# Kernel tuning notes

Measured on AMD Instinct MI355X. Metric: run time of the kernel, lower is better.

Reference implementation:

```python
import jax, jax.numpy as jnp
import numpy as np

B, S, D, H = 2, 4096, 512, 8
DK = D // H  # 64

def setup_inputs() -> dict:
    key = jax.random.key(0)
    k1, k2, k3, k4 = jax.random.split(key, 4)
    return {
        "queries": jax.random.normal(k1, (B, S, D), dtype=jnp.float32),
        "keys": jax.random.normal(k2, (B, S, D), dtype=jnp.float32),
        "values": jax.random.normal(k3, (B, S, D), dtype=jnp.float32),
        "W_o": jax.random.normal(k4, (D, D), dtype=jnp.float32) * (1.0 / np.sqrt(D)),
        "b_o": jnp.zeros((D,), dtype=jnp.float32),
    }

def reference(queries, keys, values, W_o, b_o):
    b_s, nq, _ = queries.shape
    nk = keys.shape[1]
    # split heads: (b, s, h, dk) -> (b, h, s, dk)
    q = queries.reshape(b_s, nq, H, DK).transpose(0, 2, 1, 3)
    k = keys.reshape(b_s, nk, H, DK).transpose(0, 2, 1, 3)
    v = values.reshape(b_s, nk, H, DK).transpose(0, 2, 1, 3)
    # full (nq, nk) attention matrix, scaled by sqrt(d_k)
    att = jnp.einsum("bhqd,bhkd->bhqk", q, k) / np.sqrt(DK).astype(np.float32)
    att = jax.nn.softmax(att, axis=-1)  # dropout is identity at inference
    out = jnp.einsum("bhqk,bhkd->bhqd", att, v)
    out = out.transpose(0, 2, 1, 3).reshape(b_s, nq, H * DK)
    return out @ W_o + b_o
```

## Files before the change

kernel.cpp:

```cpp
#include <hip/hip_runtime.h>
#include <hip/hip_bf16.h>

#define Bn 2
#define Sn 4096
#define Dn 512
#define Hn 8
#define DKn 64

typedef __bf16 bf16x8 __attribute__((ext_vector_type(8)));
typedef float f32x4 __attribute__((ext_vector_type(4)));

static __device__ __forceinline__ unsigned short f2bf(float x) {
    __hip_bfloat16 h = __float2bfloat16(x);
    return *reinterpret_cast<unsigned short*>(&h);
}

__global__ __launch_bounds__(256) void cvt_kernel(const float* __restrict__ in,
                                                  unsigned short* __restrict__ out, int n) {
    int i = (blockIdx.x * 256 + threadIdx.x) * 4;
    if (i < n) {
        float4 v = *(const float4*)(in + i);
        ushort4 o;
        o.x = f2bf(v.x); o.y = f2bf(v.y); o.z = f2bf(v.z); o.w = f2bf(v.w);
        *(ushort4*)(out + i) = o;
    }
}

__global__ __launch_bounds__(256) void vtrans_kernel(const float* __restrict__ V,
                                                     unsigned short* __restrict__ Vtb) {
    const int st = blockIdx.x;
    const int bh = blockIdx.y;
    const int b = bh >> 3, h = bh & 7;
    __shared__ unsigned short T[64][68];
    const int t = threadIdx.x;
    const int rlo = t >> 4;
    const int c4 = (t & 15) * 4;
    for (int i = 0; i < 4; ++i) {
        int row = rlo + i * 16;
        float4 v = *(const float4*)(V + ((size_t)(b * Sn + st * 64 + row)) * Dn + h * DKn + c4);
        T[row][c4 + 0] = f2bf(v.x); T[row][c4 + 1] = f2bf(v.y);
        T[row][c4 + 2] = f2bf(v.z); T[row][c4 + 3] = f2bf(v.w);
    }
    __syncthreads();
    for (int i = 0; i < 4; ++i) {
        int dk = rlo + i * 16;
        ushort4 o;
        o.x = T[c4 + 0][dk]; o.y = T[c4 + 1][dk]; o.z = T[c4 + 2][dk]; o.w = T[c4 + 3][dk];
        *(ushort4*)(Vtb + ((size_t)(bh * DKn + dk)) * Sn + st * 64 + c4) = o;
    }
}

__global__ __launch_bounds__(256) void wtrans_kernel(const float* __restrict__ W,
                                                     unsigned short* __restrict__ Wtb) {
    const int kt = blockIdx.x;
    const int nt = blockIdx.y;
    __shared__ unsigned short T[64][68];
    const int t = threadIdx.x;
    const int rlo = t >> 4;
    const int c4 = (t & 15) * 4;
    for (int i = 0; i < 4; ++i) {
        int row = rlo + i * 16;
        float4 v = *(const float4*)(W + (size_t)(kt * 64 + row) * Dn + nt * 64 + c4);
        T[row][c4 + 0] = f2bf(v.x); T[row][c4 + 1] = f2bf(v.y);
        T[row][c4 + 2] = f2bf(v.z); T[row][c4 + 3] = f2bf(v.w);
    }
    __syncthreads();
    for (int i = 0; i < 4; ++i) {
        int n = rlo + i * 16;
        ushort4 o;
        o.x = T[c4 + 0][n]; o.y = T[c4 + 1][n]; o.z = T[c4 + 2][n]; o.w = T[c4 + 3][n];
        *(ushort4*)(Wtb + (size_t)(nt * 64 + n) * Dn + kt * 64 + c4) = o;
    }
}

__global__ __launch_bounds__(256) void attn_kernel(
    const float* __restrict__ Q,
    const unsigned short* __restrict__ Kb,
    const unsigned short* __restrict__ Vtb,
    unsigned short* __restrict__ Ob) {
    __shared__ __align__(16) unsigned short Ksh[64 * 64];
    __shared__ __align__(16) unsigned short Vsh[64 * 64];
    __shared__ __align__(16) unsigned short Psh[4][16 * 64];

    const int qt = blockIdx.x;
    const int bh = blockIdx.y;
    const int b = bh >> 3, h = bh & 7;
    const int tid = threadIdx.x;
    const int w = tid >> 6;
    const int lane = tid & 63;
    const int l15 = lane & 15;
    const int quad = lane >> 4;
    const int q0 = qt * 64 + w * 16;
    const float cexp = 0.18033688f;

    bf16x8 qf[2];
    {
        const float* qp = Q + ((size_t)(b * Sn + q0 + l15)) * Dn + h * DKn + quad * 8;
        for (int ks = 0; ks < 2; ++ks) {
            float4 a0 = *(const float4*)(qp + ks * 32);
            float4 a1 = *(const float4*)(qp + ks * 32 + 4);
            union { unsigned short u[8]; bf16x8 v; } f;
            f.u[0] = f2bf(a0.x * cexp); f.u[1] = f2bf(a0.y * cexp);
            f.u[2] = f2bf(a0.z * cexp); f.u[3] = f2bf(a0.w * cexp);
            f.u[4] = f2bf(a1.x * cexp); f.u[5] = f2bf(a1.y * cexp);
            f.u[6] = f2bf(a1.z * cexp); f.u[7] = f2bf(a1.w * cexp);
            qf[ks] = f.v;
        }
    }

    f32x4 oacc[4];
    for (int n4 = 0; n4 < 4; ++n4)
        for (int r = 0; r < 4; ++r) oacc[n4][r] = 0.f;
    float l_ = 0.f;

    const unsigned short* Kbase = Kb + ((size_t)b * Sn) * Dn + h * DKn;
    const unsigned short* Vbase = Vtb + ((size_t)bh * DKn) * Sn;

    const int srow = tid >> 3;
    const int sch = tid & 7;

    for (int kt = 0; kt < Sn / 64; ++kt) {
        __syncthreads();
        for (int i = 0; i < 2; ++i) {
            int row = srow + i * 32;
            int sw = (sch ^ (row & 7)) * 8;
            uint4 kv = *(const uint4*)(Kbase + (size_t)(kt * 64 + row) * Dn + sch * 8);
            uint4 vv = *(const uint4*)(Vbase + (size_t)row * Sn + kt * 64 + sch * 8);
            *(uint4*)&Ksh[row * 64 + sw] = kv;
            *(uint4*)&Vsh[row * 64 + sw] = vv;
        }
        __syncthreads();

        f32x4 sacc[4];
        for (int c = 0; c < 4; ++c) {
            int kr = c * 16 + l15;
            const int sx = (kr & 7);
            bf16x8 ka0 = *(const bf16x8*)&Ksh[kr * 64 + ((quad ^ sx) * 8)];
            bf16x8 ka1 = *(const bf16x8*)&Ksh[kr * 64 + (((quad + 4) ^ sx) * 8)];
            f32x4 acc;
            for (int r = 0; r < 4; ++r) acc[r] = 0.f;
            acc = __builtin_amdgcn_mfma_f32_16x16x32_bf16(ka0, qf[0], acc, 0, 0, 0);
            acc = __builtin_amdgcn_mfma_f32_16x16x32_bf16(ka1, qf[1], acc, 0, 0, 0);
            sacc[c] = acc;
        }

        for (int c = 0; c < 4; ++c) {
            float p0 = __builtin_amdgcn_exp2f(sacc[c][0]);
            float p1 = __builtin_amdgcn_exp2f(sacc[c][1]);
            float p2 = __builtin_amdgcn_exp2f(sacc[c][2]);
            float p3 = __builtin_amdgcn_exp2f(sacc[c][3]);
            l_ += (p0 + p1) + (p2 + p3);
            ushort4 pk;
            pk.x = f2bf(p0); pk.y = f2bf(p1); pk.z = f2bf(p2); pk.w = f2bf(p3);
            int ch16 = ((quad >> 1) + 2 * c) ^ (l15 & 7);
            *(ushort4*)&Psh[w][l15 * 64 + ch16 * 8 + (quad & 1) * 4] = pk;
        }

        const int px = (l15 & 7);
        bf16x8 pb0 = *(const bf16x8*)&Psh[w][l15 * 64 + ((quad ^ px) * 8)];
        bf16x8 pb1 = *(const bf16x8*)&Psh[w][l15 * 64 + (((quad + 4) ^ px) * 8)];
        for (int n4 = 0; n4 < 4; ++n4) {
            int vr = n4 * 16 + l15;
            const int vx = (vr & 7);
            bf16x8 va0 = *(const bf16x8*)&Vsh[vr * 64 + ((quad ^ vx) * 8)];
            bf16x8 va1 = *(const bf16x8*)&Vsh[vr * 64 + (((quad + 4) ^ vx) * 8)];
            oacc[n4] = __builtin_amdgcn_mfma_f32_16x16x32_bf16(va0, pb0, oacc[n4], 0, 0, 0);
            oacc[n4] = __builtin_amdgcn_mfma_f32_16x16x32_bf16(va1, pb1, oacc[n4], 0, 0, 0);
        }
    }

    l_ += __shfl_xor(l_, 16);
    l_ += __shfl_xor(l_, 32);
    float li = 1.f / l_;
    unsigned short* op = Ob + (size_t)(b * Sn + q0 + l15) * Dn + h * DKn + quad * 4;
    for (int n4 = 0; n4 < 4; ++n4) {
        ushort4 o;
        o.x = f2bf(oacc[n4][0] * li); o.y = f2bf(oacc[n4][1] * li);
        o.z = f2bf(oacc[n4][2] * li); o.w = f2bf(oacc[n4][3] * li);
        *(ushort4*)(op + n4 * 16) = o;
    }
}

__global__ __launch_bounds__(256) void proj_kernel(
    const unsigned short* __restrict__ Ab,
    const unsigned short* __restrict__ Wtb,
    const float* __restrict__ bias,
    float* __restrict__ out) {
    __shared__ __align__(16) unsigned short Ash[64 * 64];
    __shared__ __align__(16) unsigned short Wsh[64 * 64];

    const int mt = blockIdx.x;
    const int nt = blockIdx.y;
    const int tid = threadIdx.x;
    const int w = tid >> 6;
    const int lane = tid & 63;
    const int l15 = lane & 15;
    const int quad = lane >> 4;

    f32x4 acc[4];
    for (int n4 = 0; n4 < 4; ++n4)
        for (int r = 0; r < 4; ++r) acc[n4][r] = 0.f;

    const int srow = tid >> 3;
    const int sch = tid & 7;

    for (int kt = 0; kt < Dn / 64; ++kt) {
        __syncthreads();
        for (int i = 0; i < 2; ++i) {
            int row = srow + i * 32;
            int sw = (sch ^ (row & 7)) * 8;
            *(uint4*)&Ash[row * 64 + sw] =
                *(const uint4*)(Ab + (size_t)(mt * 64 + row) * Dn + kt * 64 + sch * 8);
            *(uint4*)&Wsh[row * 64 + sw] =
                *(const uint4*)(Wtb + (size_t)(nt * 64 + row) * Dn + kt * 64 + sch * 8);
        }
        __syncthreads();

        int ar = w * 16 + l15;
        const int ax = (ar & 7);
        bf16x8 a0 = *(const bf16x8*)&Ash[ar * 64 + ((quad ^ ax) * 8)];
        bf16x8 a1 = *(const bf16x8*)&Ash[ar * 64 + (((quad + 4) ^ ax) * 8)];
        for (int n4 = 0; n4 < 4; ++n4) {
            int wr = n4 * 16 + l15;
            const int wx = (wr & 7);
            bf16x8 b0 = *(const bf16x8*)&Wsh[wr * 64 + ((quad ^ wx) * 8)];
            bf16x8 b1 = *(const bf16x8*)&Wsh[wr * 64 + (((quad + 4) ^ wx) * 8)];
            acc[n4] = __builtin_amdgcn_mfma_f32_16x16x32_bf16(a0, b0, acc[n4], 0, 0, 0);
            acc[n4] = __builtin_amdgcn_mfma_f32_16x16x32_bf16(a1, b1, acc[n4], 0, 0, 0);
        }
    }

    for (int n4 = 0; n4 < 4; ++n4) {
        int col = nt * 64 + n4 * 16 + l15;
        float bv = bias[col];
        for (int r = 0; r < 4; ++r) {
            int row = mt * 64 + w * 16 + quad * 4 + r;
            out[(size_t)row * Dn + col] = acc[n4][r] + bv;
        }
    }
}

extern "C" void kernel_launch(void* const* d_in, const int* in_sizes, int n_in,
                              void* d_out, int out_size, void* d_ws, size_t ws_size,
                              hipStream_t stream) {
    const float* Q = (const float*)d_in[0];
    const float* K = (const float*)d_in[1];
    const float* V = (const float*)d_in[2];
    const float* W = (const float*)d_in[3];
    const float* bo = (const float*)d_in[4];
    float* out = (float*)d_out;

    char* ws = (char*)d_ws;
    unsigned short* Kb  = (unsigned short*)(ws);
    unsigned short* Vtb = (unsigned short*)(ws + 8388608);
    unsigned short* Wtb = (unsigned short*)(ws + 16777216);
    unsigned short* Ob  = (unsigned short*)(ws + 17301504);

    cvt_kernel<<<4096, 256, 0, stream>>>(K, Kb, Bn * Sn * Dn);
    vtrans_kernel<<<dim3(Sn / 64, Bn * Hn), 256, 0, stream>>>(V, Vtb);
    wtrans_kernel<<<dim3(8, 8), 256, 0, stream>>>(W, Wtb);
    attn_kernel<<<dim3(Sn / 64, Bn * Hn), 256, 0, stream>>>(Q, Kb, Vtb, Ob);
    proj_kernel<<<dim3(128, 8), 256, 0, stream>>>(Ob, Wtb, bo, out);
}
```

Measured before the change: 216.9 us.

## Switch to 32x32x16 MFMA with fragment-ordered prepacked K/V/W/O layouts

Replaces the 16x16x32 MFMA tiles with 32x32x16 MFMA in both attention and projection. The prep kernels now write K, V, W and the attention output directly in per-lane MFMA fragment order, so shared-memory staging becomes contiguous copies without swizzling. P fragments are built in registers through a cross-half lane shuffle rather than a round trip through shared memory. Each attention block now covers 128 queries, which halves the block count (512 blocks) and may reduce occupancy and latency hiding. The V and W prep kernels read with strided scalar loads, which may make the prep step slower.

```diff
diff --git a/kernel.cpp b/kernel.cpp
--- a/kernel.cpp
+++ b/kernel.cpp
@@ -8,79 +8,102 @@
 #define DKn 64
 
 typedef __bf16 bf16x8 __attribute__((ext_vector_type(8)));
-typedef float f32x4 __attribute__((ext_vector_type(4)));
+typedef float f32x16 __attribute__((ext_vector_type(16)));
 
 static __device__ __forceinline__ unsigned short f2bf(float x) {
     __hip_bfloat16 h = __float2bfloat16(x);
     return *reinterpret_cast<unsigned short*>(&h);
 }
 
-__global__ __launch_bounds__(256) void cvt_kernel(const float* __restrict__ in,
-                                                  unsigned short* __restrict__ out, int n) {
-    int i = (blockIdx.x * 256 + threadIdx.x) * 4;
-    if (i < n) {
-        float4 v = *(const float4*)(in + i);
-        ushort4 o;
-        o.x = f2bf(v.x); o.y = f2bf(v.y); o.z = f2bf(v.z); o.w = f2bf(v.w);
-        *(ushort4*)(out + i) = o;
-    }
-}
-
-__global__ __launch_bounds__(256) void vtrans_kernel(const float* __restrict__ V,
-                                                     unsigned short* __restrict__ Vtb) {
-    const int st = blockIdx.x;
-    const int bh = blockIdx.y;
+static __device__ __forceinline__ uint2 pack4(float a, float b, float c, float d) {
+    union { ushort4 u; uint2 v; } r;
+    r.u.x = f2bf(a); r.u.y = f2bf(b); r.u.z = f2bf(c); r.u.w = f2bf(d);
+    return r.v;
+}
+
+static __device__ __forceinline__ bf16x8 xchg_frag(uint2 pg0, uint2 pg1, int hi) {
+    int sx = hi ? (int)pg0.x : (int)pg1.x;
+    int sy = hi ? (int)pg0.y : (int)pg1.y;
+    int rx = __shfl_xor(sx, 32);
+    int ry = __shfl_xor(sy, 32);
+    unsigned ox = hi ? pg1.x : pg0.x;
+    unsigned oy = hi ? pg1.y : pg0.y;
+    union { unsigned u[4]; bf16x8 v; } f;
+    f.u[0] = hi ? (unsigned)rx : ox;
+    f.u[1] = hi ? (unsigned)ry : oy;
+    f.u[2] = hi ? ox : (unsigned)rx;
+    f.u[3] = hi ? oy : (unsigned)ry;
+    return f.v;
+}
+
+__global__ __launch_bounds__(256) void kprep_kernel(const float* __restrict__ K,
+                                                    unsigned short* __restrict__ Kb) {
+    const int kt = blockIdx.x, bh = blockIdx.y;
     const int b = bh >> 3, h = bh & 7;
-    __shared__ unsigned short T[64][68];
-    const int t = threadIdx.x;
-    const int rlo = t >> 4;
-    const int c4 = (t & 15) * 4;
-    for (int i = 0; i < 4; ++i) {
-        int row = rlo + i * 16;
-        float4 v = *(const float4*)(V + ((size_t)(b * Sn + st * 64 + row)) * Dn + h * DKn + c4);
-        T[row][c4 + 0] = f2bf(v.x); T[row][c4 + 1] = f2bf(v.y);
-        T[row][c4 + 2] = f2bf(v.z); T[row][c4 + 3] = f2bf(v.w);
-    }
-    __syncthreads();
-    for (int i = 0; i < 4; ++i) {
-        int dk = rlo + i * 16;
-        ushort4 o;
-        o.x = T[c4 + 0][dk]; o.y = T[c4 + 1][dk]; o.z = T[c4 + 2][dk]; o.w = T[c4 + 3][dk];
-        *(ushort4*)(Vtb + ((size_t)(bh * DKn + dk)) * Sn + st * 64 + c4) = o;
-    }
-}
-
-__global__ __launch_bounds__(256) void wtrans_kernel(const float* __restrict__ W,
-                                                     unsigned short* __restrict__ Wtb) {
-    const int kt = blockIdx.x;
-    const int nt = blockIdx.y;
-    __shared__ unsigned short T[64][68];
-    const int t = threadIdx.x;
-    const int rlo = t >> 4;
-    const int c4 = (t & 15) * 4;
-    for (int i = 0; i < 4; ++i) {
-        int row = rlo + i * 16;
-        float4 v = *(const float4*)(W + (size_t)(kt * 64 + row) * Dn + nt * 64 + c4);
-        T[row][c4 + 0] = f2bf(v.x); T[row][c4 + 1] = f2bf(v.y);
-        T[row][c4 + 2] = f2bf(v.z); T[row][c4 + 3] = f2bf(v.w);
-    }
-    __syncthreads();
-    for (int i = 0; i < 4; ++i) {
-        int n = rlo + i * 16;
-        ushort4 o;
-        o.x = T[c4 + 0][n]; o.y = T[c4 + 1][n]; o.z = T[c4 + 2][n]; o.w = T[c4 + 3][n];
-        *(ushort4*)(Wtb + (size_t)(nt * 64 + n) * Dn + kt * 64 + c4) = o;
-    }
+    unsigned short* dst = Kb + ((size_t)bh * 64 + kt) * 4096;
+#pragma unroll
+    for (int i = 0; i < 2; ++i) {
+        int c = threadIdx.x + i * 256;
+        int f = c >> 6, ln = c & 63;
+        int ktile = f >> 2, ks = f & 3;
+        int row = ktile * 32 + (ln & 31);
+        int dk = ks * 16 + (ln >> 5) * 8;
+        const float* src = K + ((size_t)(b * Sn + kt * 64 + row)) * Dn + h * 64 + dk;
+        float4 a0 = *(const float4*)src;
+        float4 a1 = *(const float4*)(src + 4);
+        ushort4 o0; o0.x = f2bf(a0.x); o0.y = f2bf(a0.y); o0.z = f2bf(a0.z); o0.w = f2bf(a0.w);
+        ushort4 o1; o1.x = f2bf(a1.x); o1.y = f2bf(a1.y); o1.z = f2bf(a1.z); o1.w = f2bf(a1.w);
+        *(ushort4*)(dst + c * 8) = o0;
+        *(ushort4*)(dst + c * 8 + 4) = o1;
+    }
+}
+
+__global__ __launch_bounds__(256) void vprep_kernel(const float* __restrict__ V,
+                                                    unsigned short* __restrict__ Vb) {
+    const int kt = blockIdx.x, bh = blockIdx.y;
+    const int b = bh >> 3, h = bh & 7;
+    unsigned short* dst = Vb + ((size_t)bh * 64 + kt) * 4096;
+#pragma unroll
+    for (int i = 0; i < 2; ++i) {
+        int c = threadIdx.x + i * 256;
+        int f = c >> 6, ln = c & 63;
+        int dt = f >> 2, ks = f & 3;
+        int dk = dt * 32 + (ln & 31);
+        int key0 = ks * 16 + (ln >> 5) * 8;
+        const float* src = V + ((size_t)(b * Sn + kt * 64 + key0)) * Dn + h * 64 + dk;
+        ushort4 o0, o1;
+        o0.x = f2bf(src[0 * Dn]); o0.y = f2bf(src[1 * Dn]);
+        o0.z = f2bf(src[2 * Dn]); o0.w = f2bf(src[3 * Dn]);
+        o1.x = f2bf(src[4 * Dn]); o1.y = f2bf(src[5 * Dn]);
+        o1.z = f2bf(src[6 * Dn]); o1.w = f2bf(src[7 * Dn]);
+        *(ushort4*)(dst + c * 8) = o0;
+        *(ushort4*)(dst + c * 8 + 4) = o1;
+    }
+}
+
+__global__ __launch_bounds__(256) void wprep_kernel(const float* __restrict__ W,
+                                                    unsigned short* __restrict__ Wb) {
+    int c = blockIdx.x * 256 + threadIdx.x;
+    int ln = c & 63, f = c >> 6;
+    int ntile = f >> 5, ks = f & 31;
+    int n = ntile * 32 + (ln & 31);
+    int k0 = ks * 16 + (ln >> 5) * 8;
+    ushort4 o0, o1;
+    o0.x = f2bf(W[(size_t)(k0 + 0) * Dn + n]); o0.y = f2bf(W[(size_t)(k0 + 1) * Dn + n]);
+    o0.z = f2bf(W[(size_t)(k0 + 2) * Dn + n]); o0.w = f2bf(W[(size_t)(k0 + 3) * Dn + n]);
+    o1.x = f2bf(W[(size_t)(k0 + 4) * Dn + n]); o1.y = f2bf(W[(size_t)(k0 + 5) * Dn + n]);
+    o1.z = f2bf(W[(size_t)(k0 + 6) * Dn + n]); o1.w = f2bf(W[(size_t)(k0 + 7) * Dn + n]);
+    *(ushort4*)(Wb + c * 8) = o0;
+    *(ushort4*)(Wb + c * 8 + 4) = o1;
 }
 
 __global__ __launch_bounds__(256) void attn_kernel(
     const float* __restrict__ Q,
     const unsigned short* __restrict__ Kb,
-    const unsigned short* __restrict__ Vtb,
-    unsigned short* __restrict__ Ob) {
-    __shared__ __align__(16) unsigned short Ksh[64 * 64];
-    __shared__ __align__(16) unsigned short Vsh[64 * 64];
-    __shared__ __align__(16) unsigned short Psh[4][16 * 64];
+    const unsigned short* __restrict__ Vb,
+    unsigned short* __restrict__ ObA) {
+    __shared__ __align__(16) unsigned short Ksh[4096];
+    __shared__ __align__(16) unsigned short Vsh[4096];
 
     const int qt = blockIdx.x;
     const int bh = blockIdx.y;
@@ -88,17 +111,18 @@
     const int tid = threadIdx.x;
     const int w = tid >> 6;
     const int lane = tid & 63;
-    const int l15 = lane & 15;
-    const int quad = lane >> 4;
-    const int q0 = qt * 64 + w * 16;
+    const int q = lane & 31;
+    const int hi = lane >> 5;
+    const int q0 = qt * 128 + w * 32;
     const float cexp = 0.18033688f;
 
-    bf16x8 qf[2];
+    bf16x8 qf[4];
     {
-        const float* qp = Q + ((size_t)(b * Sn + q0 + l15)) * Dn + h * DKn + quad * 8;
-        for (int ks = 0; ks < 2; ++ks) {
-            float4 a0 = *(const float4*)(qp + ks * 32);
-            float4 a1 = *(const float4*)(qp + ks * 32 + 4);
+        const float* qp = Q + ((size_t)(b * Sn + q0 + q)) * Dn + h * 64 + hi * 8;
+#pragma unroll
+        for (int ks = 0; ks < 4; ++ks) {
+            float4 a0 = *(const float4*)(qp + ks * 16);
+            float4 a1 = *(const float4*)(qp + ks * 16 + 4);
             union { unsigned short u[8]; bf16x8 v; } f;
             f.u[0] = f2bf(a0.x * cexp); f.u[1] = f2bf(a0.y * cexp);
             f.u[2] = f2bf(a0.z * cexp); f.u[3] = f2bf(a0.w * cexp);
@@ -108,134 +132,146 @@
         }
     }
 
-    f32x4 oacc[4];
-    for (int n4 = 0; n4 < 4; ++n4)
-        for (int r = 0; r < 4; ++r) oacc[n4][r] = 0.f;
+    f32x16 oacc[2];
+#pragma unroll
+    for (int t = 0; t < 2; ++t)
+#pragma unroll
+        for (int r = 0; r < 16; ++r) oacc[t][r] = 0.f;
     float l_ = 0.f;
 
-    const unsigned short* Kbase = Kb + ((size_t)b * Sn) * Dn + h * DKn;
-    const unsigned short* Vbase = Vtb + ((size_t)bh * DKn) * Sn;
-
-    const int srow = tid >> 3;
-    const int sch = tid & 7;
-
-    for (int kt = 0; kt < Sn / 64; ++kt) {
+    const unsigned short* kg = Kb + (size_t)bh * (64 * 4096);
+    const unsigned short* vg = Vb + (size_t)bh * (64 * 4096);
+
+    for (int kt = 0; kt < 64; ++kt) {
         __syncthreads();
-        for (int i = 0; i < 2; ++i) {
-            int row = srow + i * 32;
-            int sw = (sch ^ (row & 7)) * 8;
-            uint4 kv = *(const uint4*)(Kbase + (size_t)(kt * 64 + row) * Dn + sch * 8);
-            uint4 vv = *(const uint4*)(Vbase + (size_t)row * Sn + kt * 64 + sch * 8);
-            *(uint4*)&Ksh[row * 64 + sw] = kv;
-            *(uint4*)&Vsh[row * 64 + sw] = vv;
+        {
+            const unsigned short* ks_ = kg + (size_t)kt * 4096;
+            const unsigned short* vs_ = vg + (size_t)kt * 4096;
+            uint4 k0 = *(const uint4*)(ks_ + tid * 8);
+            uint4 k1 = *(const uint4*)(ks_ + 2048 + tid * 8);
+            uint4 v0 = *(const uint4*)(vs_ + tid * 8);
+            uint4 v1 = *(const uint4*)(vs_ + 2048 + tid * 8);
+            *(uint4*)&Ksh[tid * 8] = k0;
+            *(uint4*)&Ksh[2048 + tid * 8] = k1;
+            *(uint4*)&Vsh[tid * 8] = v0;
+            *(uint4*)&Vsh[2048 + tid * 8] = v1;
         }
         __syncthreads();
 
-        f32x4 sacc[4];
-        for (int c = 0; c < 4; ++c) {
-            int kr = c * 16 + l15;
-            const int sx = (kr & 7);
-            bf16x8 ka0 = *(const bf16x8*)&Ksh[kr * 64 + ((quad ^ sx) * 8)];
-            bf16x8 ka1 = *(const bf16x8*)&Ksh[kr * 64 + (((quad + 4) ^ sx) * 8)];
-            f32x4 acc;
-            for (int r = 0; r < 4; ++r) acc[r] = 0.f;
-            acc = __builtin_amdgcn_mfma_f32_16x16x32_bf16(ka0, qf[0], acc, 0, 0, 0);
-            acc = __builtin_amdgcn_mfma_f32_16x16x32_bf16(ka1, qf[1], acc, 0, 0, 0);
-            sacc[c] = acc;
-        }
-
-        for (int c = 0; c < 4; ++c) {
-            float p0 = __builtin_amdgcn_exp2f(sacc[c][0]);
-            float p1 = __builtin_amdgcn_exp2f(sacc[c][1]);
-            float p2 = __builtin_amdgcn_exp2f(sacc[c][2]);
-            float p3 = __builtin_amdgcn_exp2f(sacc[c][3]);
-            l_ += (p0 + p1) + (p2 + p3);
-            ushort4 pk;
-            pk.x = f2bf(p0); pk.y = f2bf(p1); pk.z = f2bf(p2); pk.w = f2bf(p3);
-            int ch16 = ((quad >> 1) + 2 * c) ^ (l15 & 7);
-            *(ushort4*)&Psh[w][l15 * 64 + ch16 * 8 + (quad & 1) * 4] = pk;
-        }
-
-        const int px = (l15 & 7);
-        bf16x8 pb0 = *(const bf16x8*)&Psh[w][l15 * 64 + ((quad ^ px) * 8)];
-        bf16x8 pb1 = *(const bf16x8*)&Psh[w][l15 * 64 + (((quad + 4) ^ px) * 8)];
-        for (int n4 = 0; n4 < 4; ++n4) {
-            int vr = n4 * 16 + l15;
-            const int vx = (vr & 7);
-            bf16x8 va0 = *(const bf16x8*)&Vsh[vr * 64 + ((quad ^ vx) * 8)];
-            bf16x8 va1 = *(const bf16x8*)&Vsh[vr * 64 + (((quad + 4) ^ vx) * 8)];
-            oacc[n4] = __builtin_amdgcn_mfma_f32_16x16x32_bf16(va0, pb0, oacc[n4], 0, 0, 0);
-            oacc[n4] = __builtin_amdgcn_mfma_f32_16x16x32_bf16(va1, pb1, oacc[n4], 0, 0, 0);
-        }
-    }
-
-    l_ += __shfl_xor(l_, 16);
+        f32x16 sacc[2];
+#pragma unroll
+        for (int t = 0; t < 2; ++t)
+#pragma unroll
+            for (int r = 0; r < 16; ++r) sacc[t][r] = 0.f;
+#pragma unroll
+        for (int ks = 0; ks < 4; ++ks) {
+            bf16x8 ka0 = *(const bf16x8*)&Ksh[(0 * 4 + ks) * 512 + lane * 8];
+            bf16x8 ka1 = *(const bf16x8*)&Ksh[(1 * 4 + ks) * 512 + lane * 8];
+            sacc[0] = __builtin_amdgcn_mfma_f32_32x32x16_bf16(ka0, qf[ks], sacc[0], 0, 0, 0);
+            sacc[1] = __builtin_amdgcn_mfma_f32_32x32x16_bf16(ka1, qf[ks], sacc[1], 0, 0, 0);
+        }
+
+        float p[2][16];
+#pragma unroll
+        for (int t = 0; t < 2; ++t) {
+            float s0 = 0.f, s1 = 0.f;
+#pragma unroll
+            for (int r = 0; r < 16; r += 2) {
+                float e0 = __builtin_amdgcn_exp2f(sacc[t][r]);
+                float e1 = __builtin_amdgcn_exp2f(sacc[t][r + 1]);
+                p[t][r] = e0; p[t][r + 1] = e1;
+                s0 += e0; s1 += e1;
+            }
+            l_ += s0 + s1;
+        }
+
+#pragma unroll
+        for (int kp = 0; kp < 4; ++kp) {
+            const int c = kp >> 1, k2 = kp & 1;
+            uint2 pg0 = pack4(p[c][8 * k2 + 0], p[c][8 * k2 + 1], p[c][8 * k2 + 2], p[c][8 * k2 + 3]);
+            uint2 pg1 = pack4(p[c][8 * k2 + 4], p[c][8 * k2 + 5], p[c][8 * k2 + 6], p[c][8 * k2 + 7]);
+            bf16x8 pb = xchg_frag(pg0, pg1, hi);
+            bf16x8 va0 = *(const bf16x8*)&Vsh[(0 * 4 + kp) * 512 + lane * 8];
+            bf16x8 va1 = *(const bf16x8*)&Vsh[(1 * 4 + kp) * 512 + lane * 8];
+            oacc[0] = __builtin_amdgcn_mfma_f32_32x32x16_bf16(va0, pb, oacc[0], 0, 0, 0);
+            oacc[1] = __builtin_amdgcn_mfma_f32_32x32x16_bf16(va1, pb, oacc[1], 0, 0, 0);
+        }
+    }
+
     l_ += __shfl_xor(l_, 32);
-    float li = 1.f / l_;
-    unsigned short* op = Ob + (size_t)(b * Sn + q0 + l15) * Dn + h * DKn + quad * 4;
-    for (int n4 = 0; n4 < 4; ++n4) {
-        ushort4 o;
-        o.x = f2bf(oacc[n4][0] * li); o.y = f2bf(oacc[n4][1] * li);
-        o.z = f2bf(oacc[n4][2] * li); o.w = f2bf(oacc[n4][3] * li);
-        *(ushort4*)(op + n4 * 16) = o;
+    const float li = 1.f / l_;
+    const int gm = b * 128 + qt * 4 + w;
+#pragma unroll
+    for (int ksg = 0; ksg < 4; ++ksg) {
+        const int dt = ksg >> 1, k2 = ksg & 1;
+        uint2 pg0 = pack4(oacc[dt][8 * k2 + 0] * li, oacc[dt][8 * k2 + 1] * li,
+                          oacc[dt][8 * k2 + 2] * li, oacc[dt][8 * k2 + 3] * li);
+        uint2 pg1 = pack4(oacc[dt][8 * k2 + 4] * li, oacc[dt][8 * k2 + 5] * li,
+                          oacc[dt][8 * k2 + 6] * li, oacc[dt][8 * k2 + 7] * li);
+        bf16x8 frag = xchg_frag(pg0, pg1, hi);
+        union { bf16x8 v; uint4 u; } fu; fu.v = frag;
+        *(uint4*)&ObA[((size_t)(gm * 32 + h * 4 + ksg) * 64 + lane) * 8] = fu.u;
     }
 }
 
 __global__ __launch_bounds__(256) void proj_kernel(
-    const unsigned short* __restrict__ Ab,
-    const unsigned short* __restrict__ Wtb,
+    const unsigned short* __restrict__ ObA,
+    const unsigned short* __restrict__ Wb,
     const float* __restrict__ bias,
     float* __restrict__ out) {
-    __shared__ __align__(16) unsigned short Ash[64 * 64];
-    __shared__ __align__(16) unsigned short Wsh[64 * 64];
+    __shared__ __align__(16) unsigned short Ash[8192];
+    __shared__ __align__(16) unsigned short Wsh[4096];
 
     const int mt = blockIdx.x;
     const int nt = blockIdx.y;
     const int tid = threadIdx.x;
     const int w = tid >> 6;
     const int lane = tid & 63;
-    const int l15 = lane & 15;
-    const int quad = lane >> 4;
-
-    f32x4 acc[4];
-    for (int n4 = 0; n4 < 4; ++n4)
-        for (int r = 0; r < 4; ++r) acc[n4][r] = 0.f;
-
-    const int srow = tid >> 3;
-    const int sch = tid & 7;
-
-    for (int kt = 0; kt < Dn / 64; ++kt) {
+    const int q = lane & 31;
+    const int hi = lane >> 5;
+
+    f32x16 acc[2];
+#pragma unroll
+    for (int t = 0; t < 2; ++t)
+#pragma unroll
+        for (int r = 0; r < 16; ++r) acc[t][r] = 0.f;
+
+    for (int kt = 0; kt < 8; ++kt) {
         __syncthreads();
+#pragma unroll
+        for (int i = 0; i < 4; ++i) {
+            int ci = (tid >> 6) + i * 4;
+            int ml = ci >> 2, ksl = ci & 3;
+            *(uint4*)&Ash[ci * 512 + lane * 8] =
+                *(const uint4*)(ObA + (((size_t)(mt * 4 + ml) * 32 + kt * 4 + ksl) * 64 + lane) * 8);
+        }
+#pragma unroll
         for (int i = 0; i < 2; ++i) {
-            int row = srow + i * 32;
-            int sw = (sch ^ (row & 7)) * 8;
-            *(uint4*)&Ash[row * 64 + sw] =
-                *(const uint4*)(Ab + (size_t)(mt * 64 + row) * Dn + kt * 64 + sch * 8);
-            *(uint4*)&Wsh[row * 64 + sw] =
-                *(const uint4*)(Wtb + (size_t)(nt * 64 + row) * Dn + kt * 64 + sch * 8);
+            int ci = (tid >> 6) + i * 4;
+            int ntl = ci >> 2, ksl = ci & 3;
+            *(uint4*)&Wsh[ci * 512 + lane * 8] =
+                *(const uint4*)(Wb + (((size_t)(nt * 2 + ntl) * 32 + kt * 4 + ksl) * 64 + lane) * 8);
         }
         __syncthreads();
 
-        int ar = w * 16 + l15;
-        const int ax = (ar & 7);
-        bf16x8 a0 = *(const bf16x8*)&Ash[ar * 64 + ((quad ^ ax) * 8)];
-        bf16x8 a1 = *(const bf16x8*)&Ash[ar * 64 + (((quad + 4) ^ ax) * 8)];
-        for (int n4 = 0; n4 < 4; ++n4) {
-            int wr = n4 * 16 + l15;
-            const int wx = (wr & 7);
-            bf16x8 b0 = *(const bf16x8*)&Wsh[wr * 64 + ((quad ^ wx) * 8)];
-            bf16x8 b1 = *(const bf16x8*)&Wsh[wr * 64 + (((quad + 4) ^ wx) * 8)];
-            acc[n4] = __builtin_amdgcn_mfma_f32_16x16x32_bf16(a0, b0, acc[n4], 0, 0, 0);
-            acc[n4] = __builtin_amdgcn_mfma_f32_16x16x32_bf16(a1, b1, acc[n4], 0, 0, 0);
-        }
-    }
-
-    for (int n4 = 0; n4 < 4; ++n4) {
-        int col = nt * 64 + n4 * 16 + l15;
+#pragma unroll
+        for (int ks = 0; ks < 4; ++ks) {
+            bf16x8 a  = *(const bf16x8*)&Ash[(w * 4 + ks) * 512 + lane * 8];
+            bf16x8 b0 = *(const bf16x8*)&Wsh[(0 * 4 + ks) * 512 + lane * 8];
+            bf16x8 b1 = *(const bf16x8*)&Wsh[(4 + ks) * 512 + lane * 8];
+            acc[0] = __builtin_amdgcn_mfma_f32_32x32x16_bf16(a, b0, acc[0], 0, 0, 0);
+            acc[1] = __builtin_amdgcn_mfma_f32_32x32x16_bf16(a, b1, acc[1], 0, 0, 0);
+        }
+    }
+
+#pragma unroll
+    for (int ntl = 0; ntl < 2; ++ntl) {
+        int col = nt * 64 + ntl * 32 + q;
         float bv = bias[col];
-        for (int r = 0; r < 4; ++r) {
-            int row = mt * 64 + w * 16 + quad * 4 + r;
-            out[(size_t)row * Dn + col] = acc[n4][r] + bv;
+#pragma unroll
+        for (int reg = 0; reg < 16; ++reg) {
+            int row = mt * 128 + w * 32 + (reg & 3) + 8 * (reg >> 2) + 4 * hi;
+            out[(size_t)row * Dn + col] = acc[ntl][reg] + bv;
         }
     }
 }
@@ -252,13 +288,13 @@
 
     char* ws = (char*)d_ws;
     unsigned short* Kb  = (unsigned short*)(ws);
-    unsigned short* Vtb = (unsigned short*)(ws + 8388608);
-    unsigned short* Wtb = (unsigned short*)(ws + 16777216);
-    unsigned short* Ob  = (unsigned short*)(ws + 17301504);
-
-    cvt_kernel<<<4096, 256, 0, stream>>>(K, Kb, Bn * Sn * Dn);
-    vtrans_kernel<<<dim3(Sn / 64, Bn * Hn), 256, 0, stream>>>(V, Vtb);
-    wtrans_kernel<<<dim3(8, 8), 256, 0, stream>>>(W, Wtb);
-    attn_kernel<<<dim3(Sn / 64, Bn * Hn), 256, 0, stream>>>(Q, Kb, Vtb, Ob);
-    proj_kernel<<<dim3(128, 8), 256, 0, stream>>>(Ob, Wtb, bo, out);
-}
+    unsigned short* Vb  = (unsigned short*)(ws + 8388608);
+    unsigned short* Wb  = (unsigned short*)(ws + 16777216);
+    unsigned short* ObA = (unsigned short*)(ws + 17301504);
+
+    kprep_kernel<<<dim3(64, 16), 256, 0, stream>>>(K, Kb);
+    vprep_kernel<<<dim3(64, 16), 256, 0, stream>>>(V, Vb);
+    wprep_kernel<<<128, 256, 0, stream>>>(W, Wb);
+    attn_kernel<<<dim3(32, 16), 256, 0, stream>>>(Q, Kb, Vb, ObA);
+    proj_kernel<<<dim3(64, 8), 256, 0, stream>>>(ObA, Wb, bo, out);
+}
```

Measured after the change: 218.2 us. About the same (+0.6%).
